# Kernel optimization log

Measured on AMD Instinct MI355X. Metric: run time of the kernel, lower is better.

## Reference

```python
import jax, jax.numpy as jnp
import numpy as np

B, S, E = 2, 2048, 1024
NH, NKV = 16, 4
HD = E // NH
GS = NH // NKV


def setup_inputs() -> dict:
    key = jax.random.key(0)
    ks = jax.random.split(key, 8)
    sc = 0.02
    query = jax.random.normal(ks[0], (B, S, E), dtype=jnp.float32)
    key_t = jax.random.normal(ks[1], (B, S, E), dtype=jnp.float32)
    value = jax.random.normal(ks[2], (B, S, E), dtype=jnp.float32)
    # causal mask, broadcast shape [1,1,S,S] as in source (unsqueeze(0).unsqueeze(0))
    attn_mask = jnp.tril(jnp.ones((S, S), dtype=bool))[None, None]
    Wq = jax.random.normal(ks[3], (NH * HD, E), dtype=jnp.float32) * sc
    Wk = jax.random.normal(ks[4], (NKV * HD, E), dtype=jnp.float32) * sc
    Wv = jax.random.normal(ks[5], (NKV * HD, E), dtype=jnp.float32) * sc
    Wo = jax.random.normal(ks[6], (E, NH * HD), dtype=jnp.float32) * sc
    return {"query": query, "key": key_t, "value": value, "attn_mask": attn_mask,
            "Wq": Wq, "Wk": Wk, "Wv": Wv, "Wo": Wo}


def reference(query, key, value, attn_mask, Wq, Wk, Wv, Wo):
    # projections (nn.Linear, bias=False: y = x @ W.T)
    q = (query @ Wq.T).reshape(B, S, NH, HD).transpose(0, 2, 1, 3)   # [B,NH,S,HD]
    k = (key @ Wk.T).reshape(B, S, NKV, HD).transpose(0, 2, 1, 3)    # [B,NKV,S,HD]
    v = (value @ Wv.T).reshape(B, S, NKV, HD).transpose(0, 2, 1, 3)  # [B,NKV,S,HD]
    # repeat_interleave over head dim to match query heads
    k = jnp.repeat(k, GS, axis=1)  # [B,NH,S,HD]
    v = jnp.repeat(v, GS, axis=1)
    scale = 1.0 / np.sqrt(HD).astype(np.float32)
    scores = jnp.einsum('bhqd,bhkd->bhqk', q, k) * scale  # [B,NH,S,S]
    scores = jnp.where(attn_mask, scores, -jnp.inf)
    weights = jax.nn.softmax(scores, axis=-1)
    out = jnp.einsum('bhqk,bhkd->bhqd', weights, v)        # [B,NH,S,HD]
    out = out.transpose(0, 2, 1, 3).reshape(B, S, NH * HD)
    return out @ Wo.T  # [B,S,E]
```

## Files before the change

### kernel.cpp

```cpp
#include <hip/hip_runtime.h>
#include <hip/hip_bf16.h>

typedef __attribute__((ext_vector_type(8))) short bf16x8;
typedef __attribute__((ext_vector_type(4))) float f32x4;

#define MFMA16(a, b, c) __builtin_amdgcn_mfma_f32_16x16x32_bf16((a), (b), (c), 0, 0, 0)
#define ASYNC16(g, l)                                                     \
    __builtin_amdgcn_global_load_lds(                                     \
        (const __attribute__((address_space(1))) void*)(g),               \
        (__attribute__((address_space(3))) void*)(l), 16, 0, 0)

constexpr int B_ = 2, S_ = 2048, E_ = 1024, NH_ = 16, NKV_ = 4, HD_ = 64;

__global__ __launch_bounds__(256) void cvt_all(
    const float* __restrict__ s0, const float* __restrict__ s1,
    const float* __restrict__ s2, const float* __restrict__ s3,
    const float* __restrict__ s4, const float* __restrict__ s5,
    const float* __restrict__ s6,
    __hip_bfloat16* __restrict__ d0, __hip_bfloat16* __restrict__ d1,
    __hip_bfloat16* __restrict__ d2, __hip_bfloat16* __restrict__ d3,
    __hip_bfloat16* __restrict__ d4, __hip_bfloat16* __restrict__ d5,
    __hip_bfloat16* __restrict__ d6)
{
    const float* s;
    __hip_bfloat16* d;
    int nb;
    switch (blockIdx.y) {
        case 0: s = s0; d = d0; nb = 2048; break;
        case 1: s = s1; d = d1; nb = 2048; break;
        case 2: s = s2; d = d2; nb = 2048; break;
        case 3: s = s3; d = d3; nb = 512;  break;
        case 4: s = s4; d = d4; nb = 512;  break;
        case 5: s = s5; d = d5; nb = 128;  break;
        default: s = s6; d = d6; nb = 128; break;
    }
    if ((int)blockIdx.x >= nb) return;
    const size_t i = ((size_t)blockIdx.x * 256 + threadIdx.x) * 8;
    const float4 f0 = *reinterpret_cast<const float4*>(s + i);
    const float4 f1 = *reinterpret_cast<const float4*>(s + i + 4);
    union { __hip_bfloat16 h[8]; uint4 u; } t;
    t.h[0] = __float2bfloat16(f0.x); t.h[1] = __float2bfloat16(f0.y);
    t.h[2] = __float2bfloat16(f0.z); t.h[3] = __float2bfloat16(f0.w);
    t.h[4] = __float2bfloat16(f1.x); t.h[5] = __float2bfloat16(f1.y);
    t.h[6] = __float2bfloat16(f1.z); t.h[7] = __float2bfloat16(f1.w);
    *reinterpret_cast<uint4*>(d + i) = t.u;
}

__device__ __forceinline__ void gemm_core(
    const __hip_bfloat16* __restrict__ A,
    const __hip_bfloat16* __restrict__ W,
    void* __restrict__ C,
    const int N, const int mode, const int m0, const int n0,
    __hip_bfloat16* sA, __hip_bfloat16* sW)
{
    const int tid  = threadIdx.x;
    const int l    = tid & 63;
    const int w    = tid >> 6;
    const int quad = l >> 4;
    const int lan  = l & 15;
    const int wm   = (w >> 1) * 64;
    const int wn   = (w & 1) * 64;

    const int srow  = w * 8 + (l >> 3);
    const int scolL = (l & 7) * 8;
    const int scolG = ((l & 7) ^ (l >> 3)) * 8;

    f32x4 acc[4][4] = {};

#define STAGE(buf, kb)                                                    \
    {                                                                     \
        _Pragma("unroll")                                                 \
        for (int q = 0; q < 4; ++q) {                                     \
            const int r_ = q * 32 + srow;                                 \
            ASYNC16(A + (size_t)(m0 + r_) * E_ + (kb) + scolG,            \
                    sA + (buf) * 8192 + r_ * 64 + scolL);                 \
            ASYNC16(W + (size_t)(n0 + r_) * E_ + (kb) + scolG,            \
                    sW + (buf) * 8192 + r_ * 64 + scolL);                 \
        }                                                                 \
    }

    STAGE(0, 0)
    int cur = 0;
#pragma unroll 1
    for (int t = 0; t < 16; ++t) {
        __syncthreads();
        if (t < 15) STAGE(cur ^ 1, (t + 1) * 64)

#pragma unroll
        for (int kk = 0; kk < 2; ++kk) {
            bf16x8 af[4], bf[4];
            const int ca = ((kk * 4 + quad) ^ (lan & 7)) * 8;
#pragma unroll
            for (int i = 0; i < 4; ++i)
                af[i] = *reinterpret_cast<const bf16x8*>(
                    sA + cur * 8192 + (wm + i * 16 + lan) * 64 + ca);
#pragma unroll
            for (int j = 0; j < 4; ++j)
                bf[j] = *reinterpret_cast<const bf16x8*>(
                    sW + cur * 8192 + (wn + j * 16 + lan) * 64 + ca);
#pragma unroll
            for (int i = 0; i < 4; ++i)
#pragma unroll
                for (int j = 0; j < 4; ++j)
                    acc[i][j] = MFMA16(af[i], bf[j], acc[i][j]);
        }
        cur ^= 1;
    }
#undef STAGE

#pragma unroll
    for (int i = 0; i < 4; ++i)
#pragma unroll
        for (int j = 0; j < 4; ++j)
#pragma unroll
            for (int r = 0; r < 4; ++r) {
                const int gm = m0 + wm + i * 16 + quad * 4 + r;
                const int gn = n0 + wn + j * 16 + lan;
                const float v = acc[i][j][r];
                if (mode == 2) {
                    ((float*)C)[(size_t)gm * N + gn] = v;
                } else {
                    const __hip_bfloat16 hv = __float2bfloat16(v);
                    if (mode == 0)
                        ((__hip_bfloat16*)C)[(size_t)gm * N + gn] = hv;
                    else
                        ((__hip_bfloat16*)C)
                            [((size_t)(gm >> 11) * N + gn) * (size_t)S_ +
                             (gm & 2047)] = hv;
                }
            }
}

__global__ __launch_bounds__(256) void gemm_qkv(
    const __hip_bfloat16* __restrict__ qb, const __hip_bfloat16* __restrict__ kb,
    const __hip_bfloat16* __restrict__ vb, const __hip_bfloat16* __restrict__ Wqb,
    const __hip_bfloat16* __restrict__ Wkb, const __hip_bfloat16* __restrict__ Wvb,
    __hip_bfloat16* __restrict__ QO, __hip_bfloat16* __restrict__ Kws,
    __hip_bfloat16* __restrict__ VT)
{
    __shared__ __hip_bfloat16 sA[2 * 8192];
    __shared__ __hip_bfloat16 sW[2 * 8192];
    int id = blockIdx.x;
    const __hip_bfloat16 *A, *W;
    void* C;
    int N, mode, bx, by;
    if (id < 256)      { A = qb; W = Wqb; C = QO;  N = 1024; mode = 0; bx = id & 7; by = id >> 3; }
    else if (id < 320) { id -= 256; A = kb; W = Wkb; C = Kws; N = 256; mode = 0; bx = id & 1; by = id >> 1; }
    else               { id -= 320; A = vb; W = Wvb; C = VT;  N = 256; mode = 1; bx = id & 1; by = id >> 1; }
    gemm_core(A, W, C, N, mode, by * 128, bx * 128, sA, sW);
}

__global__ __launch_bounds__(256) void gemm_out(
    const __hip_bfloat16* __restrict__ QO, const __hip_bfloat16* __restrict__ Wob,
    float* __restrict__ out)
{
    __shared__ __hip_bfloat16 sA[2 * 8192];
    __shared__ __hip_bfloat16 sW[2 * 8192];
    const int id = blockIdx.x;
    gemm_core(QO, Wob, out, 1024, 2, (id >> 3) * 128, (id & 7) * 128, sA, sW);
}

__global__ __launch_bounds__(256) void attn(
    __hip_bfloat16* QO,
    const __hip_bfloat16* __restrict__ Kp,
    const __hip_bfloat16* __restrict__ VT)
{
    __shared__ __hip_bfloat16 sK[64][72];
    __shared__ __hip_bfloat16 sV[64][72];

    const int bx   = blockIdx.x;
    const int h    = blockIdx.y;
    const int b    = blockIdx.z;
    const int hk   = h >> 2;
    const int tid  = threadIdx.x;
    const int l    = tid & 63;
    const int w    = tid >> 6;
    const int quad = l >> 4;
    const int lan  = l & 15;
    const bool hi  = quad >= 2;
    const float KSC = 0.125f * 1.44269504088896340736f;

    const int idxA = (((quad & 1) * 32) + lan) * 4;
    const int idxB = idxA + 64;

    const int kr = tid >> 2;
    const int kc = (tid & 3) * 16;
    const __hip_bfloat16* kg =
        Kp + ((size_t)((b * S_ + kr) * NKV_) + hk) * HD_ + kc;
    const __hip_bfloat16* vg =
        VT + ((size_t)((b * NKV_ + hk) * HD_) + kr) * S_ + kc;
    const size_t kstride = (size_t)64 * NKV_ * HD_;

    for (int half = 0; half < 2; ++half) {
        const int qt  = half ? (31 - bx) : bx;
        const int qr0 = qt * 64 + w * 16;
        const int qme = qr0 + lan;

        const __hip_bfloat16* qp =
            QO + ((size_t)((b * S_ + qme) * NH_) + h) * HD_ + quad * 8;
        const bf16x8 aq0 = *reinterpret_cast<const bf16x8*>(qp);
        const bf16x8 aq1 = *reinterpret_cast<const bf16x8*>(qp + 32);

        float m_i = -3.0e38f, l_i = 0.f;
        f32x4 acc_o[4] = {};

        uint4 kv0 = *reinterpret_cast<const uint4*>(kg);
        uint4 kv1 = *reinterpret_cast<const uint4*>(kg + 8);
        uint4 vv0 = *reinterpret_cast<const uint4*>(vg);
        uint4 vv1 = *reinterpret_cast<const uint4*>(vg + 8);

        for (int kt = 0; kt <= qt; ++kt) {
            __syncthreads();
            *reinterpret_cast<uint4*>(&sK[kr][kc])     = kv0;
            *reinterpret_cast<uint4*>(&sK[kr][kc + 8]) = kv1;
            *reinterpret_cast<uint4*>(&sV[kr][kc])     = vv0;
            *reinterpret_cast<uint4*>(&sV[kr][kc + 8]) = vv1;
            __syncthreads();

            if (kt < qt) {
                const __hip_bfloat16* kn = kg + (size_t)(kt + 1) * kstride;
                const __hip_bfloat16* vn = vg + (size_t)(kt + 1) * 64;
                kv0 = *reinterpret_cast<const uint4*>(kn);
                kv1 = *reinterpret_cast<const uint4*>(kn + 8);
                vv0 = *reinterpret_cast<const uint4*>(vn);
                vv1 = *reinterpret_cast<const uint4*>(vn + 8);
            }

            f32x4 accs[4] = {};
#pragma unroll
            for (int j = 0; j < 4; ++j) {
                bf16x8 bk0 = *reinterpret_cast<const bf16x8*>(&sK[j * 16 + lan][quad * 8]);
                accs[j] = MFMA16(bk0, aq0, accs[j]);
                bf16x8 bk1 = *reinterpret_cast<const bf16x8*>(&sK[j * 16 + lan][32 + quad * 8]);
                accs[j] = MFMA16(bk1, aq1, accs[j]);
            }

            if (kt == qt) {
#pragma unroll
                for (int j = 0; j < 4; ++j)
#pragma unroll
                    for (int r = 0; r < 4; ++r) {
                        const int kcg = kt * 64 + j * 16 + quad * 4 + r;
                        if (kcg > qme) accs[j][r] = -1e30f;
                    }
            }

            float tm = accs[0][0];
#pragma unroll
            for (int j = 0; j < 4; ++j)
#pragma unroll
                for (int r = 0; r < 4; ++r) tm = fmaxf(tm, accs[j][r]);
            tm = fmaxf(tm, __shfl_xor(tm, 16));
            tm = fmaxf(tm, __shfl_xor(tm, 32));
            const float mnew  = fmaxf(m_i, tm);
            const float alpha = exp2f((m_i - mnew) * KSC);
            float ps = 0.f;
#pragma unroll
            for (int j = 0; j < 4; ++j)
#pragma unroll
                for (int r = 0; r < 4; ++r) {
                    const float p = exp2f((accs[j][r] - mnew) * KSC);
                    accs[j][r] = p;
                    ps += p;
                }
            ps += __shfl_xor(ps, 16);
            ps += __shfl_xor(ps, 32);
            l_i = l_i * alpha + ps;
            m_i = mnew;
#pragma unroll
            for (int dd = 0; dd < 4; ++dd)
#pragma unroll
                for (int r = 0; r < 4; ++r) acc_o[dd][r] *= alpha;

            uint pk[4][2];
#pragma unroll
            for (int j = 0; j < 4; ++j)
#pragma unroll
                for (int hh = 0; hh < 2; ++hh) {
                    union { __hip_bfloat16 bh[2]; uint u; } t;
                    t.bh[0] = __float2bfloat16(accs[j][2 * hh]);
                    t.bh[1] = __float2bfloat16(accs[j][2 * hh + 1]);
                    pk[j][hh] = t.u;
                }

#pragma unroll
            for (int kk = 0; kk < 2; ++kk) {
                union { uint u[4]; bf16x8 v; } pb;
#pragma unroll
                for (int w2 = 0; w2 < 4; ++w2) {
                    const int idx = (w2 & 2) ? idxB : idxA;
                    const uint a = (uint)__builtin_amdgcn_ds_bpermute(
                        idx, (int)pk[2 * kk][w2 & 1]);
                    const uint bb = (uint)__builtin_amdgcn_ds_bpermute(
                        idx, (int)pk[2 * kk + 1][w2 & 1]);
                    pb.u[w2] = hi ? bb : a;
                }
#pragma unroll
                for (int dd = 0; dd < 4; ++dd) {
                    bf16x8 av = *reinterpret_cast<const bf16x8*>(
                        &sV[dd * 16 + lan][kk * 32 + quad * 8]);
                    acc_o[dd] = MFMA16(av, pb.v, acc_o[dd]);
                }
            }
        }

        const float inv = 1.0f / l_i;
        __hip_bfloat16* op =
            QO + ((size_t)((b * S_ + qme) * NH_) + h) * HD_ + quad * 4;
#pragma unroll
        for (int dd = 0; dd < 4; ++dd) {
            union { __hip_bfloat16 bh[4]; uint2 u; } t;
#pragma unroll
            for (int r = 0; r < 4; ++r)
                t.bh[r] = __float2bfloat16(acc_o[dd][r] * inv);
            *reinterpret_cast<uint2*>(op + dd * 16) = t.u;
        }
    }
}

extern "C" void kernel_launch(void* const* d_in, const int* in_sizes, int n_in,
                              void* d_out, int out_size, void* d_ws, size_t ws_size,
                              hipStream_t stream) {
    const float* q  = (const float*)d_in[0];
    const float* k  = (const float*)d_in[1];
    const float* v  = (const float*)d_in[2];
    const float* Wq = (const float*)d_in[4];
    const float* Wk = (const float*)d_in[5];
    const float* Wv = (const float*)d_in[6];
    const float* Wo = (const float*)d_in[7];

    __hip_bfloat16* ws = (__hip_bfloat16*)d_ws;
    __hip_bfloat16* qb   = ws;
    __hip_bfloat16* kb   = qb  + 4194304;
    __hip_bfloat16* vb   = kb  + 4194304;
    __hip_bfloat16* QO   = vb  + 4194304;
    __hip_bfloat16* Kws  = QO  + 4194304;
    __hip_bfloat16* VT   = Kws + 1048576;
    __hip_bfloat16* Wqb  = VT  + 1048576;
    __hip_bfloat16* Wob  = Wqb + 1048576;
    __hip_bfloat16* Wkb  = Wob + 1048576;
    __hip_bfloat16* Wvb  = Wkb + 262144;

    cvt_all<<<dim3(2048, 7), 256, 0, stream>>>(
        q, k, v, Wq, Wo, Wk, Wv, qb, kb, vb, Wqb, Wob, Wkb, Wvb);

    gemm_qkv<<<dim3(384), 256, 0, stream>>>(
        qb, kb, vb, Wqb, Wkb, Wvb, QO, Kws, VT);

    attn<<<dim3(16, NH_, B_), 256, 0, stream>>>(QO, Kws, VT);

    gemm_out<<<dim3(256), 256, 0, stream>>>(QO, Wob, (float*)d_out);
}
```

Measured before the change: 220.5 us.

## Rework attention: one q-tile per block, XOR-swizzled LDS, lazy rescale, compact convert grid

The attention kernel now launches one block per query tile, heaviest tiles first, instead of pairing two tiles per block. This doubles the grid and uses the scheduler for load balancing. K/V shared tiles drop their padding and use an XOR swizzle to avoid bank conflicts. MFMA sections are raised with s_setprio, and the online softmax skips the rescale unless the running max grows by more than a threshold. The convert kernel uses a flat 1D grid so no blocks are launched idle. The lazy rescale keeps values bounded but adds a wave-wide vote, and the finer grid trades the built-in load pairing for more blocks.

```diff
diff --git a/kernel.cpp b/kernel.cpp
--- a/kernel.cpp
+++ b/kernel.cpp
@@ -22,20 +22,20 @@
     __hip_bfloat16* __restrict__ d4, __hip_bfloat16* __restrict__ d5,
     __hip_bfloat16* __restrict__ d6)
 {
+    int id = blockIdx.x;
     const float* s;
     __hip_bfloat16* d;
-    int nb;
-    switch (blockIdx.y) {
-        case 0: s = s0; d = d0; nb = 2048; break;
-        case 1: s = s1; d = d1; nb = 2048; break;
-        case 2: s = s2; d = d2; nb = 2048; break;
-        case 3: s = s3; d = d3; nb = 512;  break;
-        case 4: s = s4; d = d4; nb = 512;  break;
-        case 5: s = s5; d = d5; nb = 128;  break;
-        default: s = s6; d = d6; nb = 128; break;
-    }
-    if ((int)blockIdx.x >= nb) return;
-    const size_t i = ((size_t)blockIdx.x * 256 + threadIdx.x) * 8;
+    if (id < 6144) {
+        const int which = id >> 11;
+        s = which == 0 ? s0 : (which == 1 ? s1 : s2);
+        d = which == 0 ? d0 : (which == 1 ? d1 : d2);
+        id &= 2047;
+    } else if (id < 6656) { s = s3; d = d3; id -= 6144; }
+    else if (id < 7168)   { s = s4; d = d4; id -= 6656; }
+    else if (id < 7296)   { s = s5; d = d5; id -= 7168; }
+    else                  { s = s6; d = d6; id -= 7296; }
+
+    const size_t i = ((size_t)id * 256 + threadIdx.x) * 8;
     const float4 f0 = *reinterpret_cast<const float4*>(s + i);
     const float4 f1 = *reinterpret_cast<const float4*>(s + i + 4);
     union { __hip_bfloat16 h[8]; uint4 u; } t;
@@ -165,10 +165,10 @@
     const __hip_bfloat16* __restrict__ Kp,
     const __hip_bfloat16* __restrict__ VT)
 {
-    __shared__ __hip_bfloat16 sK[64][72];
-    __shared__ __hip_bfloat16 sV[64][72];
-
-    const int bx   = blockIdx.x;
+    __shared__ __hip_bfloat16 sK[64][64];
+    __shared__ __hip_bfloat16 sV[64][64];
+
+    const int qt   = 31 - blockIdx.x;
     const int h    = blockIdx.y;
     const int b    = blockIdx.z;
     const int hk   = h >> 2;
@@ -183,138 +183,151 @@
     const int idxA = (((quad & 1) * 32) + lan) * 4;
     const int idxB = idxA + 64;
 
-    const int kr = tid >> 2;
-    const int kc = (tid & 3) * 16;
+    const int kr  = tid >> 2;
+    const int s0c = (tid & 3) * 2;
+    const int sw0 = (s0c ^ (kr & 7)) * 8;
+    const int sw1 = ((s0c + 1) ^ (kr & 7)) * 8;
+    const int kc  = s0c * 8;
+
     const __hip_bfloat16* kg =
         Kp + ((size_t)((b * S_ + kr) * NKV_) + hk) * HD_ + kc;
     const __hip_bfloat16* vg =
         VT + ((size_t)((b * NKV_ + hk) * HD_) + kr) * S_ + kc;
     const size_t kstride = (size_t)64 * NKV_ * HD_;
 
-    for (int half = 0; half < 2; ++half) {
-        const int qt  = half ? (31 - bx) : bx;
-        const int qr0 = qt * 64 + w * 16;
-        const int qme = qr0 + lan;
-
-        const __hip_bfloat16* qp =
-            QO + ((size_t)((b * S_ + qme) * NH_) + h) * HD_ + quad * 8;
-        const bf16x8 aq0 = *reinterpret_cast<const bf16x8*>(qp);
-        const bf16x8 aq1 = *reinterpret_cast<const bf16x8*>(qp + 32);
-
-        float m_i = -3.0e38f, l_i = 0.f;
-        f32x4 acc_o[4] = {};
-
-        uint4 kv0 = *reinterpret_cast<const uint4*>(kg);
-        uint4 kv1 = *reinterpret_cast<const uint4*>(kg + 8);
-        uint4 vv0 = *reinterpret_cast<const uint4*>(vg);
-        uint4 vv1 = *reinterpret_cast<const uint4*>(vg + 8);
-
-        for (int kt = 0; kt <= qt; ++kt) {
-            __syncthreads();
-            *reinterpret_cast<uint4*>(&sK[kr][kc])     = kv0;
-            *reinterpret_cast<uint4*>(&sK[kr][kc + 8]) = kv1;
-            *reinterpret_cast<uint4*>(&sV[kr][kc])     = vv0;
-            *reinterpret_cast<uint4*>(&sV[kr][kc + 8]) = vv1;
-            __syncthreads();
-
-            if (kt < qt) {
-                const __hip_bfloat16* kn = kg + (size_t)(kt + 1) * kstride;
-                const __hip_bfloat16* vn = vg + (size_t)(kt + 1) * 64;
-                kv0 = *reinterpret_cast<const uint4*>(kn);
-                kv1 = *reinterpret_cast<const uint4*>(kn + 8);
-                vv0 = *reinterpret_cast<const uint4*>(vn);
-                vv1 = *reinterpret_cast<const uint4*>(vn + 8);
-            }
-
-            f32x4 accs[4] = {};
-#pragma unroll
-            for (int j = 0; j < 4; ++j) {
-                bf16x8 bk0 = *reinterpret_cast<const bf16x8*>(&sK[j * 16 + lan][quad * 8]);
-                accs[j] = MFMA16(bk0, aq0, accs[j]);
-                bf16x8 bk1 = *reinterpret_cast<const bf16x8*>(&sK[j * 16 + lan][32 + quad * 8]);
-                accs[j] = MFMA16(bk1, aq1, accs[j]);
-            }
-
-            if (kt == qt) {
-#pragma unroll
-                for (int j = 0; j < 4; ++j)
-#pragma unroll
-                    for (int r = 0; r < 4; ++r) {
-                        const int kcg = kt * 64 + j * 16 + quad * 4 + r;
-                        if (kcg > qme) accs[j][r] = -1e30f;
-                    }
-            }
-
-            float tm = accs[0][0];
+    const int qr0 = qt * 64 + w * 16;
+    const int qme = qr0 + lan;
+
+    const __hip_bfloat16* qp =
+        QO + ((size_t)((b * S_ + qme) * NH_) + h) * HD_ + quad * 8;
+    const bf16x8 aq0 = *reinterpret_cast<const bf16x8*>(qp);
+    const bf16x8 aq1 = *reinterpret_cast<const bf16x8*>(qp + 32);
+
+    float m_i = -3.0e38f, l_i = 0.f;
+    f32x4 acc_o[4] = {};
+
+    uint4 kv0 = *reinterpret_cast<const uint4*>(kg);
+    uint4 kv1 = *reinterpret_cast<const uint4*>(kg + 8);
+    uint4 vv0 = *reinterpret_cast<const uint4*>(vg);
+    uint4 vv1 = *reinterpret_cast<const uint4*>(vg + 8);
+
+    for (int kt = 0; kt <= qt; ++kt) {
+        __syncthreads();
+        *reinterpret_cast<uint4*>(&sK[kr][sw0]) = kv0;
+        *reinterpret_cast<uint4*>(&sK[kr][sw1]) = kv1;
+        *reinterpret_cast<uint4*>(&sV[kr][sw0]) = vv0;
+        *reinterpret_cast<uint4*>(&sV[kr][sw1]) = vv1;
+        __syncthreads();
+
+        if (kt < qt) {
+            const __hip_bfloat16* kn = kg + (size_t)(kt + 1) * kstride;
+            const __hip_bfloat16* vn = vg + (size_t)(kt + 1) * 64;
+            kv0 = *reinterpret_cast<const uint4*>(kn);
+            kv1 = *reinterpret_cast<const uint4*>(kn + 8);
+            vv0 = *reinterpret_cast<const uint4*>(vn);
+            vv1 = *reinterpret_cast<const uint4*>(vn + 8);
+        }
+
+        f32x4 accs[4] = {};
+        __builtin_amdgcn_s_setprio(1);
+#pragma unroll
+        for (int j = 0; j < 4; ++j) {
+            const int swq0 = (quad ^ (lan & 7)) * 8;
+            const int swq1 = ((4 + quad) ^ (lan & 7)) * 8;
+            bf16x8 bk0 = *reinterpret_cast<const bf16x8*>(&sK[j * 16 + lan][swq0]);
+            accs[j] = MFMA16(bk0, aq0, accs[j]);
+            bf16x8 bk1 = *reinterpret_cast<const bf16x8*>(&sK[j * 16 + lan][swq1]);
+            accs[j] = MFMA16(bk1, aq1, accs[j]);
+        }
+        __builtin_amdgcn_s_setprio(0);
+
+        if (kt == qt) {
 #pragma unroll
             for (int j = 0; j < 4; ++j)
 #pragma unroll
-                for (int r = 0; r < 4; ++r) tm = fmaxf(tm, accs[j][r]);
-            tm = fmaxf(tm, __shfl_xor(tm, 16));
-            tm = fmaxf(tm, __shfl_xor(tm, 32));
+                for (int r = 0; r < 4; ++r) {
+                    const int kcg = kt * 64 + j * 16 + quad * 4 + r;
+                    if (kcg > qme) accs[j][r] = -1e30f;
+                }
+        }
+
+        float tm = accs[0][0];
+#pragma unroll
+        for (int j = 0; j < 4; ++j)
+#pragma unroll
+            for (int r = 0; r < 4; ++r) tm = fmaxf(tm, accs[j][r]);
+        tm = fmaxf(tm, __shfl_xor(tm, 16));
+        tm = fmaxf(tm, __shfl_xor(tm, 32));
+
+        if (__any((tm - m_i) * KSC > 8.0f)) {
             const float mnew  = fmaxf(m_i, tm);
             const float alpha = exp2f((m_i - mnew) * KSC);
-            float ps = 0.f;
-#pragma unroll
-            for (int j = 0; j < 4; ++j)
-#pragma unroll
-                for (int r = 0; r < 4; ++r) {
-                    const float p = exp2f((accs[j][r] - mnew) * KSC);
-                    accs[j][r] = p;
-                    ps += p;
-                }
-            ps += __shfl_xor(ps, 16);
-            ps += __shfl_xor(ps, 32);
-            l_i = l_i * alpha + ps;
-            m_i = mnew;
+            l_i *= alpha;
+            m_i  = mnew;
 #pragma unroll
             for (int dd = 0; dd < 4; ++dd)
 #pragma unroll
                 for (int r = 0; r < 4; ++r) acc_o[dd][r] *= alpha;
-
-            uint pk[4][2];
-#pragma unroll
-            for (int j = 0; j < 4; ++j)
-#pragma unroll
-                for (int hh = 0; hh < 2; ++hh) {
-                    union { __hip_bfloat16 bh[2]; uint u; } t;
-                    t.bh[0] = __float2bfloat16(accs[j][2 * hh]);
-                    t.bh[1] = __float2bfloat16(accs[j][2 * hh + 1]);
-                    pk[j][hh] = t.u;
-                }
-
-#pragma unroll
-            for (int kk = 0; kk < 2; ++kk) {
-                union { uint u[4]; bf16x8 v; } pb;
-#pragma unroll
-                for (int w2 = 0; w2 < 4; ++w2) {
-                    const int idx = (w2 & 2) ? idxB : idxA;
-                    const uint a = (uint)__builtin_amdgcn_ds_bpermute(
-                        idx, (int)pk[2 * kk][w2 & 1]);
-                    const uint bb = (uint)__builtin_amdgcn_ds_bpermute(
-                        idx, (int)pk[2 * kk + 1][w2 & 1]);
-                    pb.u[w2] = hi ? bb : a;
-                }
-#pragma unroll
-                for (int dd = 0; dd < 4; ++dd) {
-                    bf16x8 av = *reinterpret_cast<const bf16x8*>(
-                        &sV[dd * 16 + lan][kk * 32 + quad * 8]);
-                    acc_o[dd] = MFMA16(av, pb.v, acc_o[dd]);
-                }
-            }
-        }
-
-        const float inv = 1.0f / l_i;
-        __hip_bfloat16* op =
-            QO + ((size_t)((b * S_ + qme) * NH_) + h) * HD_ + quad * 4;
-#pragma unroll
-        for (int dd = 0; dd < 4; ++dd) {
-            union { __hip_bfloat16 bh[4]; uint2 u; } t;
-#pragma unroll
-            for (int r = 0; r < 4; ++r)
-                t.bh[r] = __float2bfloat16(acc_o[dd][r] * inv);
-            *reinterpret_cast<uint2*>(op + dd * 16) = t.u;
-        }
+        }
+
+        float ps = 0.f;
+#pragma unroll
+        for (int j = 0; j < 4; ++j)
+#pragma unroll
+            for (int r = 0; r < 4; ++r) {
+                const float p = exp2f((accs[j][r] - m_i) * KSC);
+                accs[j][r] = p;
+                ps += p;
+            }
+        ps += __shfl_xor(ps, 16);
+        ps += __shfl_xor(ps, 32);
+        l_i += ps;
+
+        uint pk[4][2];
+#pragma unroll
+        for (int j = 0; j < 4; ++j)
+#pragma unroll
+            for (int hh = 0; hh < 2; ++hh) {
+                union { __hip_bfloat16 bh[2]; uint u; } t;
+                t.bh[0] = __float2bfloat16(accs[j][2 * hh]);
+                t.bh[1] = __float2bfloat16(accs[j][2 * hh + 1]);
+                pk[j][hh] = t.u;
+            }
+
+#pragma unroll
+        for (int kk = 0; kk < 2; ++kk) {
+            union { uint u[4]; bf16x8 v; } pb;
+#pragma unroll
+            for (int w2 = 0; w2 < 4; ++w2) {
+                const int idx = (w2 & 2) ? idxB : idxA;
+                const uint a = (uint)__builtin_amdgcn_ds_bpermute(
+                    idx, (int)pk[2 * kk][w2 & 1]);
+                const uint bb = (uint)__builtin_amdgcn_ds_bpermute(
+                    idx, (int)pk[2 * kk + 1][w2 & 1]);
+                pb.u[w2] = hi ? bb : a;
+            }
+            __builtin_amdgcn_s_setprio(1);
+#pragma unroll
+            for (int dd = 0; dd < 4; ++dd) {
+                const int swv = ((kk * 4 + quad) ^ (lan & 7)) * 8;
+                bf16x8 av = *reinterpret_cast<const bf16x8*>(
+                    &sV[dd * 16 + lan][swv]);
+                acc_o[dd] = MFMA16(av, pb.v, acc_o[dd]);
+            }
+            __builtin_amdgcn_s_setprio(0);
+        }
+    }
+
+    const float inv = 1.0f / l_i;
+    __hip_bfloat16* op =
+        QO + ((size_t)((b * S_ + qme) * NH_) + h) * HD_ + quad * 4;
+#pragma unroll
+    for (int dd = 0; dd < 4; ++dd) {
+        union { __hip_bfloat16 bh[4]; uint2 u; } t;
+#pragma unroll
+        for (int r = 0; r < 4; ++r)
+            t.bh[r] = __float2bfloat16(acc_o[dd][r] * inv);
+        *reinterpret_cast<uint2*>(op + dd * 16) = t.u;
     }
 }
 
@@ -341,13 +354,13 @@
     __hip_bfloat16* Wkb  = Wob + 1048576;
     __hip_bfloat16* Wvb  = Wkb + 262144;
 
-    cvt_all<<<dim3(2048, 7), 256, 0, stream>>>(
+    cvt_all<<<dim3(7424), 256, 0, stream>>>(
         q, k, v, Wq, Wo, Wk, Wv, qb, kb, vb, Wqb, Wob, Wkb, Wvb);
 
     gemm_qkv<<<dim3(384), 256, 0, stream>>>(
         qb, kb, vb, Wqb, Wkb, Wvb, QO, Kws, VT);
 
-    attn<<<dim3(16, NH_, B_), 256, 0, stream>>>(QO, Kws, VT);
+    attn<<<dim3(32, NH_, B_), 256, 0, stream>>>(QO, Kws, VT);
 
     gemm_out<<<dim3(256), 256, 0, stream>>>(QO, Wob, (float*)d_out);
 }
```

Measured after the change: 242.8 us. 10.1% more time.
